# Performance work log

Hardware: AMD Instinct MI355X
Metric: run time of the kernel (lower is better)

## Reference

```python
import jax, jax.numpy as jnp
import numpy as np

WINDOW = 32


def _dilate(mask, iters=5):
    # scipy binary_dilation with default cross structure, `iters` iterations
    m = mask.copy()
    for _ in range(iters):
        d = m.copy()
        d[1:, :] |= m[:-1, :]
        d[:-1, :] |= m[1:, :]
        d[:, 1:] |= m[:, :-1]
        d[:, :-1] |= m[:, 1:]
        m = d
    return m


def _label8(mask):
    # skimage measure.label, default 8-connectivity, via min-label propagation
    h, w = mask.shape
    lab = np.where(mask, np.arange(1, mask.size + 1, dtype=np.int64).reshape(h, w), 0)
    BIG = mask.size + 2
    while True:
        p = np.pad(np.where(mask, lab, BIG), 1, constant_values=BIG)
        m = np.full((h, w), BIG, dtype=np.int64)
        for dy in (-1, 0, 1):
            for dx in (-1, 0, 1):
                m = np.minimum(m, p[1 + dy:1 + dy + h, 1 + dx:1 + dx + w])
        new = np.where(mask, m, 0)
        if np.array_equal(new, lab):
            break
        lab = new
    u = np.unique(lab)
    out = np.searchsorted(u, lab)
    if u[0] != 0:
        out = out + 1
    return out


def _malis(seg_flat, e1, e2, costs, pos):
    # MALIS edge weights: Kruskal on descending affinities with union-find;
    # pos=True counts same-(nonzero)-label pairs merged by each edge,
    # pos=False counts cross-label pairs between labeled nodes.
    n = seg_flat.size
    parent = np.arange(n)
    cnt = [dict() for _ in range(n)]
    for i in range(n):
        s = int(seg_flat[i])
        if s != 0:
            cnt[i][s] = 1
    w = np.zeros(costs.shape[0], np.float32)

    def find(x):
        r = x
        while parent[r] != r:
            r = parent[r]
        while parent[x] != r:
            parent[x], x = r, parent[x]
        return r

    order = np.argsort(-costs, kind='stable')
    for ei in order:
        ra, rb = find(int(e1[ei])), find(int(e2[ei]))
        if ra == rb:
            continue
        ca, cb = cnt[ra], cnt[rb]
        small, large = (ca, cb) if len(ca) <= len(cb) else (cb, ca)
        same = 0
        for kk, v in small.items():
            same += v * large.get(kk, 0)
        if pos:
            w[ei] = same
        else:
            sa = sum(ca.values())
            sb = sum(cb.values())
            w[ei] = sa * sb - same
        parent[rb] = ra
        for kk, v in cb.items():
            ca[kk] = ca.get(kk, 0) + v
        cnt[rb] = None
    return w


def compute_malis_weights(pred_np, target_np):
    B, C, H, W = pred_np.shape
    wn_full = np.zeros(pred_np.shape, np.float32)
    wp_full = np.zeros(pred_np.shape, np.float32)
    win = WINDOW
    idx = np.arange(win * win).reshape(win, win)
    e1 = np.concatenate([idx[:, :-1].ravel(), idx[:-1, :].ravel()])
    e2 = np.concatenate([idx[:, 1:].ravel(), idx[1:, :].ravel()])
    for k in range(H // win):
        for j in range(W // win):
            p = pred_np[:, :, k * win:(k + 1) * win, j * win:(j + 1) * win]
            t = target_np[:, :, k * win:(k + 1) * win, j * win:(j + 1) * win]
            costs = np.concatenate([
                (p[:, :, :, :-1] + p[:, :, :, 1:]).reshape(B, -1),
                (p[:, :, :-1, :] + p[:, :, 1:, :]).reshape(B, -1)], axis=1).astype(np.float32)
            gtc = np.concatenate([
                (t[:, :, :, :-1] + t[:, :, :, 1:]).reshape(B, -1),
                (t[:, :, :-1, :] + t[:, :, 1:, :]).reshape(B, -1)], axis=1).astype(np.float32)
            costs_n = costs.copy()
            costs_p = costs.copy()
            costs_n[gtc > 20] = 20
            costs_p[gtc < 10] = 0
            gtc = np.minimum(gtc, 20)
            for i in range(B):
                sg = _label8(_dilate(t[i, 0] == 0, 5) == 0)
                en = _malis(sg.ravel(), e1, e2, costs_n[i], False)
                ep = _malis(sg.ravel(), e1, e2, costs_p[i], True)
                sn = en.sum()
                if sn > 0:
                    en = en / sn
                sp = ep.sum()
                if sp > 0:
                    ep = ep / sp
                en[gtc[i] >= 10] = 0
                ep[gtc[i] < 20] = 0
                for ew, out in ((en, wn_full), (ep, wp_full)):
                    wh, wv = np.split(ew, 2)
                    wh = wh.reshape(win, win - 1)
                    wv = wv.reshape(win - 1, win)
                    nodes = np.zeros((win, win), np.float32)
                    nodes[:, :-1] += wh
                    nodes[:, 1:] += wh
                    nodes[:-1, :] += wv
                    nodes[1:, :] += wv
                    out[i, 0, k * win:(k + 1) * win, j * win:(j + 1) * win] = nodes
    return wn_full, wp_full


def setup_inputs() -> dict:
    key = jax.random.key(0)
    k1, k2 = jax.random.split(key)
    pred = jax.random.uniform(k1, (2, 1, 256, 256), jnp.float32) * 20.0
    target = jax.random.randint(k2, (2, 1, 256, 256), 0, 26).astype(jnp.float32)
    return {"pred": pred, "target": target, "malis_lr": 1.0, "malis_lr_pos": 1.0}


def reference(pred, target, malis_lr, malis_lr_pos):
    # weights are computed from detached values (CPU graph algorithm), constants wrt autodiff
    wn, wp = compute_malis_weights(np.asarray(pred), np.asarray(target))
    wn = jnp.asarray(wn, jnp.float32)
    wp = jnp.asarray(wp, jnp.float32)
    loss = malis_lr * jnp.square(pred) * wn + malis_lr_pos * jnp.square(20.0 - pred) * wp
    return loss.sum()
```

## Files before the change

### kernel.cpp

```cpp
#include <hip/hip_runtime.h>
#include <cstdint>

#define NPIX  1024
#define NH    992
#define NEDGE 1984
#define NSORT 2048
#define NGRP  31
#define HFS   4300
#define POOLN (NPIX + 2*HFS)

typedef unsigned long long u64;
typedef unsigned int u32;

static __device__ __forceinline__ u64 packRoot(int sL,int off,int len,int cap){
    return (u64)(u32)(sL & 0x7FF) | ((u64)(u32)(off & 0x3FFF) << 11) |
           ((u64)(u32)(len & 0x7FF) << 25) | ((u64)(u32)(cap & 0x7FF) << 36);
}
#define R_SL(R)  ((int)((R) & 0x7FF))
#define R_OFF(R) ((int)(((R)>>11) & 0x3FFF))
#define R_LEN(R) ((int)(((R)>>25) & 0x7FF))
#define R_CAP(R) ((int)(((R)>>36) & 0x7FF))
#define EMASK 0x3FFFFFFu

static __device__ __forceinline__ int rdl(int v, int l){ return __builtin_amdgcn_readlane(v, l); }

static __device__ __forceinline__ u64 sxor64(u64 v, int m){
    u32 lo = (u32)__shfl_xor((int)(v & 0xFFFFFFFFull), m, 64);
    u32 hi = (u32)__shfl_xor((int)(v >> 32), m, 64);
    return ((u64)hi << 32) | lo;
}

static __device__ __forceinline__ void edgeAB(int e, int &a, int &b){
    if (e < NH) { int r = (int)((unsigned)e / 31u); a = e + r; b = a + 1; }
    else        { a = e - NH; b = a + 32; }
}

#define CE(x, y, up) { u64 _a=(x), _b=(y); bool _lt=(_a<_b); \
    u64 _mn=_lt?_a:_b, _mx=_lt?_b:_a; (x)=(up)?_mn:_mx; (y)=(up)?_mx:_mn; }
#define CEX(x, xm, keepmin) { u64 _p=sxor64((x),(xm)); bool _lt=((x)<_p); \
    u64 _mn=_lt?(x):_p, _mx=_lt?_p:(x); (x)=(keepmin)?_mn:_mx; }

static __device__ __forceinline__ int wredi(int v){
    #pragma unroll
    for (int o = 32; o > 0; o >>= 1) v += __shfl_xor(v, o, 64);
    return v;
}
static __device__ __forceinline__ float wredf(float v){
    #pragma unroll
    for (int o = 32; o > 0; o >>= 1) v += __shfl_xor(v, o, 64);
    return v;
}

__global__ __launch_bounds__(128) void malis_kernel(
    const float* __restrict__ pred,
    const float* __restrict__ target,
    const float* __restrict__ lr_p,
    const float* __restrict__ lrp_p,
    float* __restrict__ out)
{
    const int tid  = threadIdx.x;
    const int lane = tid & 63;
    const int wv   = tid >> 6;
    const int bid  = blockIdx.x;
    const int bb   = bid >> 6;
    const int win  = bid & 63;
    const int wy   = win >> 3, wx = win & 7;
    const int base = bb * 65536 + (wy * 32) * 256 + wx * 32;

    __shared__ __align__(16) u32 Ks[2][NSORT];
    __shared__ u64   root[2][NPIX];
    __shared__ float predL[NPIX];
    __shared__ float costs[NEDGE];
    __shared__ u32   poolS[2][POOLN];
    __shared__ unsigned short Q[2][NPIX];
    __shared__ float Qw[2][NPIX];
    __shared__ u32   claimS[2][NPIX];
    __shared__ short seg[NPIX];
    __shared__ short par[2][NPIX];
    __shared__ short H[2][NPIX + 1];
    __shared__ unsigned char tgtL[NPIX];
    __shared__ unsigned char gtcL[NEDGE];
    __shared__ u32   rowmaskL[32];
    __shared__ u32   fgL[32];
    __shared__ unsigned short baseL[33];
    __shared__ int   flags[2];

    u32* runPar = (u32*)poolS;
    unsigned short* labIdRun = (unsigned short*)(runPar + 512);

    for (int j = 0; j < 8; ++j) {
        int i = tid + 128 * j;
        int r = i >> 5, c = i & 31;
        float pv = pred[base + r * 256 + c];
        float tv = target[base + r * 256 + c];
        predL[i] = pv;
        tgtL[i]  = (unsigned char)tv;
        u64 zb = __ballot(tv == 0.0f);
        if (lane == 0) {
            int rr = 4 * j + 2 * wv;
            rowmaskL[rr]     = (u32)zb;
            rowmaskL[rr + 1] = (u32)(zb >> 32);
        }
    }
    if (tid == 0) flags[1] = 0;
    for (int x = tid; x < 512; x += 128) runPar[x] = (u32)x;
    __syncthreads();

    if (tid < 32) {
        u32 m = rowmaskL[tid];
        #pragma unroll
        for (int it = 0; it < 5; ++it) {
            u32 um = __shfl(m, (tid == 0) ? 0 : tid - 1, 64);
            if (tid == 0) um = 0;
            u32 dm = __shfl(m, (tid == 31) ? 31 : tid + 1, 64);
            if (tid == 31) dm = 0;
            m = m | (m << 1) | (m >> 1) | um | dm;
        }
        u32 f = ~m;
        fgL[tid] = f;
        int ns = __popc(f & ~(f << 1));
        int x = ns;
        #pragma unroll
        for (int off = 1; off < 32; off <<= 1) {
            int y = __shfl(x, (tid >= off) ? tid - off : 0, 64);
            if (tid >= off) x += y;
        }
        baseL[tid] = (unsigned short)(x - ns);
        if (tid == 31) baseL[32] = (unsigned short)x;
    }
    __syncthreads();
    const int nRuns = (int)baseL[32];

    for (;;) {
        if (tid == 0) flags[0] = 0;
        __syncthreads();
        bool chg = false;
        for (int j = 0; j < 8; ++j) {
            int i = tid + 128 * j;
            int r = i >> 5, c = i & 31;
            if (r == 0) continue;
            u32 fr = fgL[r];
            if (!((fr >> c) & 1u)) continue;
            u32 fu = fgL[r - 1];
            u32 nb = fu & (u32)((7ull << c) >> 1);
            if (!nb) continue;
            u32 Sr = fr & ~(fr << 1);
            int a = (int)baseL[r] + __popc(Sr & ((2u << c) - 1u)) - 1;
            for (;;) { int p = (int)runPar[a]; if (p == a) break; a = p; }
            u32 Su = fu & ~(fu << 1);
            int bu = (int)baseL[r - 1];
            while (nb) {
                int cc = __ffs((int)nb) - 1; nb &= nb - 1;
                int b = bu + __popc(Su & ((2u << cc) - 1u)) - 1;
                for (;;) { int p = (int)runPar[b]; if (p == b) break; b = p; }
                if (a != b) {
                    int mnr = a < b ? a : b;
                    int mxr = a ^ b ^ mnr;
                    atomicMin(&runPar[mxr], (u32)mnr);
                    chg = true;
                    a = mnr;
                }
            }
        }
        if (chg) flags[0] = 1;
        __syncthreads();
        if (!flags[0]) break;
        for (int x = tid; x < nRuns; x += 128) {
            u32 p = runPar[x];
            runPar[x] = runPar[p];
        }
        __syncthreads();
    }

    for (int x = tid; x < nRuns; x += 128)
        if ((int)runPar[x] == x) labIdRun[x] = (unsigned short)atomicAdd(&flags[1], 1);
    __syncthreads();

    for (int j = 0; j < 8; ++j) {
        int i = tid + 128 * j;
        int r = i >> 5, c = i & 31;
        u32 fr = fgL[r];
        short s = 0;
        if ((fr >> c) & 1u) {
            u32 Sr = fr & ~(fr << 1);
            int x = (int)baseL[r] + __popc(Sr & ((2u << c) - 1u)) - 1;
            for (;;) { int p = (int)runPar[x]; if (p == x) break; x = p; }
            s = (short)((int)labIdRun[x] + 1);
        }
        seg[i] = s;
    }

    for (int e = tid; e < NEDGE; e += 128) {
        int a, b2; edgeAB(e, a, b2);
        costs[e] = predL[a] + predL[b2];
        gtcL[e]  = (unsigned char)(tgtL[a] + tgtL[b2]);
    }
    __syncthreads();

    const int ph = wv;
    u32*   Ks_   = Ks[ph];
    short* par_  = par[ph];
    u64*   root_ = root[ph];
    u32*   pool_ = poolS[ph];
    short* H_    = H[ph];
    unsigned short* Q_ = Q[ph];
    float* Qw_   = Qw[ph];
    u32*   claim_= claimS[ph];

    u64 sk[32];
    #pragma unroll
    for (int r = 0; r < 32; ++r) {
        int e = lane * 32 + r;
        u64 kv = ~0ULL;
        if (e < NEDGE) {
            float cv = costs[e];
            int g = gtcL[e];
            if (ph == 0) { if (g > 20) cv = 20.0f; }
            else         { if (g < 10) cv = 0.0f; }
            kv = (((u64)(~__float_as_uint(cv))) << 32) | (u32)e;
        }
        sk[r] = kv;
    }
    #pragma unroll
    for (int kk2 = 2; kk2 <= 32; kk2 <<= 1) {
        #pragma unroll
        for (int j = kk2 >> 1; j > 0; j >>= 1) {
            #pragma unroll
            for (int r = 0; r < 32; ++r) {
                if ((r & j) == 0) {
                    bool up = (kk2 == 32) ? ((lane & 1) == 0) : ((r & kk2) == 0);
                    CE(sk[r], sk[r | j], up);
                }
            }
        }
    }
    #pragma unroll
    for (int kk2 = 64; kk2 <= 2048; kk2 <<= 1) {
        const bool up = ((lane & (kk2 >> 5)) == 0);
        #pragma unroll
        for (int j = kk2 >> 1; j >= 32; j >>= 1) {
            const int xm = j >> 5;
            const bool keepmin = (((lane & xm) == 0) == up);
            #pragma unroll
            for (int r = 0; r < 32; ++r) { CEX(sk[r], xm, keepmin); }
        }
        #pragma unroll
        for (int j = 16; j > 0; j >>= 1) {
            #pragma unroll
            for (int r = 0; r < 32; ++r) {
                if ((r & j) == 0) { CE(sk[r], sk[r | j], up); }
            }
        }
    }
    #pragma unroll
    for (int r = 0; r < 32; r += 4) {
        uint4 v4;
        v4.x = (u32)sk[r]; v4.y = (u32)sk[r+1]; v4.z = (u32)sk[r+2]; v4.w = (u32)sk[r+3];
        *(uint4*)&Ks_[lane * 32 + r] = v4;
    }

    for (int i = lane; i < NPIX; i += 64) {
        short s2 = seg[i];
        par_[i] = (short)(i | (s2 ? 0x8000 : 0));
        root_[i] = s2 ? ((1ull << 62) | ((u32)(unsigned short)s2 << 16) | 1u) : 0ull;
        H_[i] = 0;
        claim_[i] = ~0u;
    }
    if (lane == 0) H_[NPIX] = 0;
    __builtin_amdgcn_wave_barrier();

    const u64 ltm = (1ull << lane) - 1;
    u32 bump = NPIX;
    u32 halfEnd = NPIX + HFS;
    int curHalf = 0;

    auto do_gc = [&]() {
        u32 tgt = (curHalf == 0) ? (u32)(NPIX + HFS) : (u32)NPIX;
        u32 nb = tgt;
        for (int c = 0; c < 16; ++c) {
            int i0 = c * 64 + lane;
            u64 Ri = root_[i0];
            bool live = (Ri != 0) && ((Ri >> 62) == 0);
            u64 rbm = __ballot(live);
            while (rbm) {
                int j = __ffsll(rbm) - 1; rbm &= rbm - 1;
                int r = c * 64 + j;
                u64 R = root_[r];
                int len = R_LEN(R);
                int off = R_OFF(R);
                for (int t = lane; t < len; t += 64) {
                    u32 v2 = pool_[off + t];
                    pool_[nb + t] = v2;
                }
                __builtin_amdgcn_wave_barrier();
                if (lane == 0) root_[r] = packRoot(R_SL(R), (int)nb, len, len);
                nb += (u32)len;
            }
        }
        bump = nb;
        halfEnd = tgt + HFS;
        curHalf ^= 1;
    };

    int qn = 0;
    u32 rnd = 1;
    int curE = (int)Ks_[lane];
    for (int g2 = 0; g2 < NGRP; ++g2) {
        int nextE = (g2 + 1 < NGRP) ? (int)Ks_[(g2 + 1) * 64 + lane] : 0;
        const int myE = curE;
        int ea, eb2; edgeAB(myE, ea, eb2);
        int ra = ea, rb = eb2;
        int laA, laB;
        for (;;) {
            int va = (int)(unsigned short)par_[ra];
            int vb = (int)(unsigned short)par_[rb];
            int pa = va & 0x3FF, pb = vb & 0x3FF;
            bool fa = (pa != ra), fb = (pb != rb);
            if (!fa && !fb) { laA = va >> 15; laB = vb >> 15; break; }
            int ga = (int)(unsigned short)par_[pa];
            int gb = (int)(unsigned short)par_[pb];
            if (fa) { par_[ra] = (short)ga; ra = ga & 0x3FF; }
            if (fb) { par_[rb] = (short)gb; rb = gb & 0x3FF; }
        }
        bool alive = (ra != rb);

        for (;;) {
            if (!__ballot(alive)) break;
            const bool av = alive;
            const u32 tag = ((0x03FFFFFFu - rnd) << 6) | (u32)lane;
            ++rnd;
            int mn = ra < rb ? ra : rb;
            int mx = ra ^ rb ^ mn;
            int winner = (laA == laB) ? mn : (laA ? ra : rb);
            int loser  = (laA == laB) ? mx : (laA ? rb : ra);
            bool wgt = (laA & laB) != 0;
            if (av)        atomicMin(&claim_[loser],  tag);
            if (av && wgt) atomicMin(&claim_[winner], tag);
            bool sel = false;
            if (av) {
                u32 cl = claim_[loser];
                u32 cw = wgt ? claim_[winner] : tag;
                sel = (cl == tag) && (cw == tag);
            }
            u64 wm = __ballot(sel && wgt);
            int qidx = qn + (int)__popcll(wm & ltm);
            qn += (int)__popcll(wm);
            if (sel) par_[loser] = (short)winner;

            bool needPool = false;
            if (sel && wgt) {
                u64 RW = root_[mn], RL = root_[mx];
                int tW = (int)(RW >> 62), tL2 = (int)(RL >> 62);
                if (tW != 0 && tL2 != 0) {
                    u32 a0 = (u32)RW & EMASK, a1 = (u32)(RW >> 26) & EMASK;
                    u32 b0 = (u32)RL & EMASK, b1 = (u32)(RL >> 26) & EMASK;
                    u32 la0 = a0 >> 16, la1 = a1 >> 16;
                    u32 lb0 = b0 >> 16, lb1 = b1 >> 16;
                    int ca0 = (int)(a0 & 0xFFFF), ca1 = (int)(a1 & 0xFFFF);
                    int cb0 = (int)(b0 & 0xFFFF), cb1 = (int)(b1 & 0xFFFF);
                    int sLa = ca0 + ((tW == 2) ? ca1 : 0);
                    int sLb = cb0 + ((tL2 == 2) ? cb1 : 0);
                    int same = 0;
                    if (lb0 == la0) same += ca0 * cb0;
                    else if (tW == 2 && lb0 == la1) same += ca1 * cb0;
                    if (tL2 == 2) {
                        if (lb1 == la0) same += ca0 * cb1;
                        else if (tW == 2 && lb1 == la1) same += ca1 * cb1;
                    }
                    u32 r0 = a0, r1 = (tW == 2) ? a1 : 0;
                    int n = tW; bool ovf = false;
                    if (lb0 == la0) r0 += (u32)cb0;
                    else if (tW == 2 && lb0 == la1) r1 += (u32)cb0;
                    else { if (n == 1) { r1 = b0; n = 2; } else ovf = true; }
                    if (tL2 == 2) {
                        if (lb1 == la0) r0 += (u32)cb1;
                        else if (tW == 2 && lb1 == la1) r1 += (u32)cb1;
                        else { if (n == 1) { r1 = b1; n = 2; } else ovf = true; }
                    }
                    if (!ovf) {
                        root_[mn] = ((u64)(u32)n << 62) | ((u64)r1 << 26) | r0;
                        root_[mx] = 0;
                        Qw_[qidx] = (float)(ph ? same : (sLa * sLb - same));
                        Q_[qidx]  = (unsigned short)myE;
                    } else needPool = true;
                } else needPool = true;
            }

            u64 pm = __ballot(needPool);
            while (pm) {
                int f = __ffsll(pm) - 1; pm &= pm - 1;
                int A  = rdl(mn, f),  B  = rdl(mx, f);
                int e  = rdl(myE, f), qi = rdl(qidx, f);
                u64 RA = root_[A], RB = root_[B];
                int tA = (int)(RA >> 62), tB = (int)(RB >> 62);
                int lenA = tA ? tA : R_LEN(RA);
                int lenB = tB ? tB : R_LEN(RB);
                if (bump + (u32)(lenA + lenB + 8) > halfEnd) {
                    do_gc();
                    RA = root_[A]; RB = root_[B];
                    tA = (int)(RA >> 62); tB = (int)(RB >> 62);
                    lenA = tA ? tA : R_LEN(RA);
                    lenB = tB ? tB : R_LEN(RB);
                }
                int sLa, sLb;
                int offA = 0, capA = 0, offB = 0, capB = 0;
                if (tA == 0) { sLa = R_SL(RA); offA = R_OFF(RA); capA = R_CAP(RA); }
                else {
                    u32 a0 = (u32)RA & EMASK, a1 = (u32)(RA >> 26) & EMASK;
                    sLa = (int)(a0 & 0xFFFF) + ((tA == 2) ? (int)(a1 & 0xFFFF) : 0);
                }
                if (tB == 0) { sLb = R_SL(RB); offB = R_OFF(RB); capB = R_CAP(RB); }
                else {
                    u32 b0 = (u32)RB & EMASK, b1 = (u32)(RB >> 26) & EMASK;
                    sLb = (int)(b0 & 0xFFFF) + ((tB == 2) ? (int)(b1 & 0xFFFF) : 0);
                }
                u32 eA = 0, eB = 0;
                if (lenA <= 64) {
                    if (tA == 0) { if (lane < lenA) eA = pool_[offA + lane]; }
                    else {
                        u32 a0 = (u32)RA & EMASK, a1 = (u32)(RA >> 26) & EMASK;
                        eA = (lane == 0) ? a0 : ((lane == 1 && tA == 2) ? a1 : 0);
                    }
                }
                if (lenB <= 64) {
                    if (tB == 0) { if (lane < lenB) eB = pool_[offB + lane]; }
                    else {
                        u32 b0 = (u32)RB & EMASK, b1 = (u32)(RB >> 26) & EMASK;
                        eB = (lane == 0) ? b0 : ((lane == 1 && tB == 2) ? b1 : 0);
                    }
                }
                u32 eS, eL; int lenS, lenL, offS, offL, capL, tL;
                if (lenA <= lenB) { eS=eA; lenS=lenA; offS=offA; eL=eB; lenL=lenB; offL=offB; capL=capB; tL=tB; }
                else              { eS=eB; lenS=lenB; offS=offB; eL=eA; lenL=lenA; offL=offA; capL=capA; tL=tA; }
                int dOff, dLen, dCap;
                int same = 0;
                u64 newR;

                if (lenS + lenL <= 64) {
                    dLen = lenL;
                    for (int t = 0; t < lenS; ++t) {
                        u32 xs = (u32)rdl((int)eS, t);
                        bool match = (lane < lenL) && ((eL >> 16) == (xs >> 16));
                        u64 mb = __ballot(match);
                        if (mb) {
                            int ml = __ffsll(mb) - 1;
                            same += (int)(xs & 0xFFFF) * ((int)rdl((int)eL, ml) & 0xFFFF);
                            if (match) eL += (xs & 0xFFFF);
                        } else {
                            if (lane == dLen) eL = xs;
                            dLen++;
                        }
                    }
                    if (dLen <= 2) {
                        u32 m0 = (u32)rdl((int)eL, 0) & EMASK;
                        u32 m1 = (dLen > 1) ? ((u32)rdl((int)eL, 1) & EMASK) : 0u;
                        newR = ((u64)(u32)dLen << 62) | ((u64)m1 << 26) | m0;
                    } else {
                        if (tL == 0 && dLen <= capL) { dOff = offL; dCap = capL; }
                        else { dOff = (int)bump; dCap = (dLen + 3) & ~3; bump += (u32)dCap; }
                        if (lane < dLen) pool_[dOff + lane] = eL;
                        newR = packRoot(sLa + sLb, dOff, dLen, dCap);
                    }
                } else {
                    dOff = (int)bump;
                    dCap = (lenL + lenS + 4) & ~3; bump += (u32)dCap;
                    if (lenS <= 64) {
                        if (lane < lenS) H_[eS >> 16] = (short)(eS & 0xFFFF);
                    } else {
                        for (int j = lane; j < lenS; j += 64) {
                            u32 es = pool_[offS + j];
                            H_[es >> 16] = (short)(es & 0xFFFF);
                        }
                    }
                    __builtin_amdgcn_wave_barrier();
                    int sp = 0;
                    for (int j = lane; j < lenL; j += 64) {
                        u32 el = pool_[offL + j];
                        int h = (int)H_[el >> 16];
                        sp += h * (int)(el & 0xFFFF);
                        pool_[dOff + j] = el + (u32)h;
                        if (h) H_[el >> 16] = 0;
                    }
                    same = wredi(sp);
                    __builtin_amdgcn_wave_barrier();
                    int baseU = 0;
                    if (lenS <= 64) {
                        bool un = (lane < lenS) && (H_[eS >> 16] != 0);
                        u64 ub = __ballot(un);
                        if (un) {
                            int pos = __popcll(ub & ltm);
                            pool_[dOff + lenL + pos] = eS;
                            H_[eS >> 16] = 0;
                        }
                        baseU = (int)__popcll(ub);
                    } else {
                        for (int j0 = 0; j0 < lenS; j0 += 64) {
                            int j = j0 + lane;
                            bool un = false; u32 es = 0;
                            if (j < lenS) { es = pool_[offS + j]; un = (H_[es >> 16] != 0); }
                            u64 ub = __ballot(un);
                            if (un) {
                                int pos = __popcll(ub & ltm);
                                pool_[dOff + lenL + baseU + pos] = es;
                                H_[es >> 16] = 0;
                            }
                            baseU += (int)__popcll(ub);
                        }
                    }
                    dLen = lenL + baseU;
                    newR = packRoot(sLa + sLb, dOff, dLen, dCap);
                }
                if (lane == 0) {
                    Qw_[qi] = (float)(ph ? same : (sLa * sLb - same));
                    Q_[qi]  = (unsigned short)e;
                    root_[A] = newR;
                    root_[B] = 0;
                }
                __builtin_amdgcn_wave_barrier();
            }

            if (av) {
                for (;;) {
                    int va = (int)(unsigned short)par_[ra];
                    int vb = (int)(unsigned short)par_[rb];
                    int pa = va & 0x3FF, pb = vb & 0x3FF;
                    bool fa = (pa != ra), fb = (pb != rb);
                    if (!fa && !fb) { laA = va >> 15; laB = vb >> 15; break; }
                    int ga = (int)(unsigned short)par_[pa];
                    int gb = (int)(unsigned short)par_[pb];
                    if (fa) { par_[ra] = (short)ga; ra = ga & 0x3FF; }
                    if (fb) { par_[rb] = (short)gb; rb = gb & 0x3FF; }
                }
                alive = !sel && (ra != rb);
            }
        }
        curE = nextE;
        __builtin_amdgcn_wave_barrier();
    }

    float s_loc = 0.0f;
    for (int q = lane; q < qn; q += 64) s_loc += Qw_[q];
    const float sn = wredf(s_loc);

    const float scale = ph ? lrp_p[0] : lr_p[0];
    float acc = 0.0f;
    for (int q = lane; q < qn; q += 64) {
        float wv2 = Qw_[q];
        if (wv2 == 0.0f) continue;
        if (sn > 0.0f) wv2 /= sn;
        int me = (int)Q_[q];
        int g = gtcL[me];
        bool zero = ph ? (g < 20) : (g >= 10);
        if (zero) continue;
        int a2, b2; edgeAB(me, a2, b2);
        float pa = predL[a2], pb = predL[b2];
        float fa2, fb2;
        if (ph == 0) { fa2 = pa * pa; fb2 = pb * pb; }
        else { float qa = 20.0f - pa, qb = 20.0f - pb; fa2 = qa * qa; fb2 = qb * qb; }
        acc += scale * wv2 * (fa2 + fb2);
    }
    acc = wredf(acc);
    if (lane == 0) atomicAdd(out, acc);
}

__global__ void zero_out_kernel(float* o)
{
    if (threadIdx.x == 0 && blockIdx.x == 0) o[0] = 0.0f;
}

extern "C" void kernel_launch(void* const* d_in, const int* in_sizes, int n_in,
                              void* d_out, int out_size, void* d_ws, size_t ws_size,
                              hipStream_t stream)
{
    const float* pred   = (const float*)d_in[0];
    const float* target = (const float*)d_in[1];
    const float* lr     = (const float*)d_in[2];
    const float* lrp    = (const float*)d_in[3];
    float* out = (float*)d_out;

    zero_out_kernel<<<1, 64, 0, stream>>>(out);
    malis_kernel<<<128, 128, 0, stream>>>(pred, target, lr, lrp, out);
}
```

Measured before the change: 322.4 us.

## Split MALIS kernel into preprocessing and per-phase drain kernels

Splits the monolithic kernel into a pre_kernel that labels segments and sorts edges per window, writing them to workspace, and a drain_kernel that runs each Kruskal phase (pos/neg) in its own 64-thread block. This doubles the number of blocks (256 instead of 128) so the serial union-find phases spread over more CUs, and reduces per-block LDS. In exchange it adds a kernel launch and a global-memory round trip for labels and sorted keys. The drain reads sorted keys from global rather than LDS.

```diff
diff --git a/kernel.cpp b/kernel.cpp
--- a/kernel.cpp
+++ b/kernel.cpp
@@ -12,6 +12,9 @@
 typedef unsigned long long u64;
 typedef unsigned int u32;
 
+#define WS_SEG   0
+#define WS_KS    262144
+
 static __device__ __forceinline__ u64 packRoot(int sL,int off,int len,int cap){
     return (u64)(u32)(sL & 0x7FF) | ((u64)(u32)(off & 0x3FFF) << 11) |
            ((u64)(u32)(len & 0x7FF) << 25) | ((u64)(u32)(cap & 0x7FF) << 36);
@@ -35,6 +38,13 @@
     else        { a = e - NH; b = a + 32; }
 }
 
+static __device__ __forceinline__ int winBase(int wslot){
+    int bb = wslot >> 6;
+    int win = wslot & 63;
+    int wy = win >> 3, wx = win & 7;
+    return bb * 65536 + (wy * 32) * 256 + wx * 32;
+}
+
 #define CE(x, y, up) { u64 _a=(x), _b=(y); bool _lt=(_a<_b); \
     u64 _mn=_lt?_a:_b, _mx=_lt?_b:_a; (x)=(up)?_mn:_mx; (y)=(up)?_mx:_mn; }
 #define CEX(x, xm, keepmin) { u64 _p=sxor64((x),(xm)); bool _lt=((x)<_p); \
@@ -51,42 +61,28 @@
     return v;
 }
 
-__global__ __launch_bounds__(128) void malis_kernel(
+__global__ __launch_bounds__(128) void pre_kernel(
     const float* __restrict__ pred,
     const float* __restrict__ target,
-    const float* __restrict__ lr_p,
-    const float* __restrict__ lrp_p,
-    float* __restrict__ out)
+    unsigned short* __restrict__ segW,
+    u32* __restrict__ KsW)
 {
     const int tid  = threadIdx.x;
     const int lane = tid & 63;
     const int wv   = tid >> 6;
     const int bid  = blockIdx.x;
-    const int bb   = bid >> 6;
-    const int win  = bid & 63;
-    const int wy   = win >> 3, wx = win & 7;
-    const int base = bb * 65536 + (wy * 32) * 256 + wx * 32;
-
-    __shared__ __align__(16) u32 Ks[2][NSORT];
-    __shared__ u64   root[2][NPIX];
+    const int base = winBase(bid);
+
     __shared__ float predL[NPIX];
     __shared__ float costs[NEDGE];
-    __shared__ u32   poolS[2][POOLN];
-    __shared__ unsigned short Q[2][NPIX];
-    __shared__ float Qw[2][NPIX];
-    __shared__ u32   claimS[2][NPIX];
-    __shared__ short seg[NPIX];
-    __shared__ short par[2][NPIX];
-    __shared__ short H[2][NPIX + 1];
     __shared__ unsigned char tgtL[NPIX];
     __shared__ unsigned char gtcL[NEDGE];
     __shared__ u32   rowmaskL[32];
     __shared__ u32   fgL[32];
     __shared__ unsigned short baseL[33];
+    __shared__ u32   runPar[512];
+    __shared__ unsigned short labIdRun[512];
     __shared__ int   flags[2];
-
-    u32* runPar = (u32*)poolS;
-    unsigned short* labIdRun = (unsigned short*)(runPar + 512);
 
     for (int j = 0; j < 8; ++j) {
         int i = tid + 128 * j;
@@ -176,18 +172,19 @@
         if ((int)runPar[x] == x) labIdRun[x] = (unsigned short)atomicAdd(&flags[1], 1);
     __syncthreads();
 
+    unsigned short* segG = segW + bid * NPIX;
     for (int j = 0; j < 8; ++j) {
         int i = tid + 128 * j;
         int r = i >> 5, c = i & 31;
         u32 fr = fgL[r];
-        short s = 0;
+        unsigned short s = 0;
         if ((fr >> c) & 1u) {
             u32 Sr = fr & ~(fr << 1);
             int x = (int)baseL[r] + __popc(Sr & ((2u << c) - 1u)) - 1;
             for (;;) { int p = (int)runPar[x]; if (p == x) break; x = p; }
-            s = (short)((int)labIdRun[x] + 1);
-        }
-        seg[i] = s;
+            s = (unsigned short)((int)labIdRun[x] + 1);
+        }
+        segG[i] = s;
     }
 
     for (int e = tid; e < NEDGE; e += 128) {
@@ -198,15 +195,6 @@
     __syncthreads();
 
     const int ph = wv;
-    u32*   Ks_   = Ks[ph];
-    short* par_  = par[ph];
-    u64*   root_ = root[ph];
-    u32*   pool_ = poolS[ph];
-    short* H_    = H[ph];
-    unsigned short* Q_ = Q[ph];
-    float* Qw_   = Qw[ph];
-    u32*   claim_= claimS[ph];
-
     u64 sk[32];
     #pragma unroll
     for (int r = 0; r < 32; ++r) {
@@ -252,21 +240,59 @@
             }
         }
     }
+    u32* KsG = KsW + (size_t)(bid * 2 + ph) * NSORT;
     #pragma unroll
     for (int r = 0; r < 32; r += 4) {
         uint4 v4;
         v4.x = (u32)sk[r]; v4.y = (u32)sk[r+1]; v4.z = (u32)sk[r+2]; v4.w = (u32)sk[r+3];
-        *(uint4*)&Ks_[lane * 32 + r] = v4;
-    }
+        *(uint4*)&KsG[lane * 32 + r] = v4;
+    }
+}
+
+__global__ __launch_bounds__(64) void drain_kernel(
+    const float* __restrict__ pred,
+    const float* __restrict__ target,
+    const unsigned short* __restrict__ segW,
+    const u32* __restrict__ KsW,
+    const float* __restrict__ lr_p,
+    const float* __restrict__ lrp_p,
+    float* __restrict__ out)
+{
+    const int lane = threadIdx.x;
+    const int bid  = blockIdx.x;
+    const int ph   = bid & 1;
+    const int wslot= bid >> 1;
+    const int base = winBase(wslot);
+    const unsigned short* segG = segW + wslot * NPIX;
+    const u32* KsG = KsW + (size_t)bid * NSORT;
+
+    __shared__ u64   root_[NPIX];
+    __shared__ u32   pool_[POOLN];
+    __shared__ unsigned short Q_[NPIX];
+    __shared__ float Qw_[NPIX];
+    __shared__ u32   claim_[NPIX];
+    __shared__ short par_[NPIX];
+    __shared__ short H_[NPIX + 1];
+    __shared__ float predL[NPIX];
+    __shared__ unsigned char tgtL[NPIX];
+    __shared__ unsigned char gtcL[NEDGE];
 
     for (int i = lane; i < NPIX; i += 64) {
-        short s2 = seg[i];
+        int r = i >> 5, c = i & 31;
+        predL[i] = pred[base + r * 256 + c];
+        tgtL[i]  = (unsigned char)target[base + r * 256 + c];
+        unsigned short s2 = segG[i];
         par_[i] = (short)(i | (s2 ? 0x8000 : 0));
-        root_[i] = s2 ? ((1ull << 62) | ((u32)(unsigned short)s2 << 16) | 1u) : 0ull;
+        root_[i] = s2 ? ((1ull << 62) | ((u32)s2 << 16) | 1u) : 0ull;
         H_[i] = 0;
         claim_[i] = ~0u;
     }
     if (lane == 0) H_[NPIX] = 0;
+    __builtin_amdgcn_wave_barrier();
+    for (int e = lane; e < NEDGE; e += 64) {
+        int a, b2; edgeAB(e, a, b2);
+        gtcL[e] = (unsigned char)(tgtL[a] + tgtL[b2]);
+    }
     __builtin_amdgcn_wave_barrier();
 
     const u64 ltm = (1ull << lane) - 1;
@@ -304,9 +330,9 @@
 
     int qn = 0;
     u32 rnd = 1;
-    int curE = (int)Ks_[lane];
+    int curE = (int)KsG[lane];
     for (int g2 = 0; g2 < NGRP; ++g2) {
-        int nextE = (g2 + 1 < NGRP) ? (int)Ks_[(g2 + 1) * 64 + lane] : 0;
+        int nextE = (g2 + 1 < NGRP) ? (int)KsG[(g2 + 1) * 64 + lane] : 0;
         const int myE = curE;
         int ea, eb2; edgeAB(myE, ea, eb2);
         int ra = ea, rb = eb2;
@@ -578,6 +604,11 @@
     const float* lrp    = (const float*)d_in[3];
     float* out = (float*)d_out;
 
+    char* ws = (char*)d_ws;
+    unsigned short* segW = (unsigned short*)(ws + WS_SEG);
+    u32* KsW = (u32*)(ws + WS_KS);
+
     zero_out_kernel<<<1, 64, 0, stream>>>(out);
-    malis_kernel<<<128, 128, 0, stream>>>(pred, target, lr, lrp, out);
-}
+    pre_kernel<<<128, 128, 0, stream>>>(pred, target, segW, KsW);
+    drain_kernel<<<256, 64, 0, stream>>>(pred, target, segW, KsW, lr, lrp, out);
+}
```

Result: slower. 331.6 us (+2.9%).

## Split pos/neg MALIS phases into separate single-wave blocks

Applied to the files above, without the earlier changes.

Each 128-thread block previously ran both phases (one per wave) after a shared labeling preamble; now each phase runs in its own 64-thread block, giving 256 blocks. The labeling preamble uses wave barriers and ballots instead of __syncthreads and shared flags, with label ids assigned by ballot prefix counts. This spreads work across more CUs and removes block-level syncs, but the labeling and edge-cost preamble is now computed twice per window by a single wave.

```diff
diff --git a/kernel.cpp b/kernel.cpp
--- a/kernel.cpp
+++ b/kernel.cpp
@@ -35,6 +35,13 @@
     else        { a = e - NH; b = a + 32; }
 }
 
+static __device__ __forceinline__ int winBase(int wslot){
+    int bb = wslot >> 6;
+    int win = wslot & 63;
+    int wy = win >> 3, wx = win & 7;
+    return bb * 65536 + (wy * 32) * 256 + wx * 32;
+}
+
 #define CE(x, y, up) { u64 _a=(x), _b=(y); bool _lt=(_a<_b); \
     u64 _mn=_lt?_a:_b, _mx=_lt?_b:_a; (x)=(up)?_mn:_mx; (y)=(up)?_mx:_mn; }
 #define CEX(x, xm, keepmin) { u64 _p=sxor64((x),(xm)); bool _lt=((x)<_p); \
@@ -51,92 +58,85 @@
     return v;
 }
 
-__global__ __launch_bounds__(128) void malis_kernel(
+__global__ __launch_bounds__(64) void malis_kernel(
     const float* __restrict__ pred,
     const float* __restrict__ target,
     const float* __restrict__ lr_p,
     const float* __restrict__ lrp_p,
     float* __restrict__ out)
 {
-    const int tid  = threadIdx.x;
-    const int lane = tid & 63;
-    const int wv   = tid >> 6;
+    const int lane = threadIdx.x;
     const int bid  = blockIdx.x;
-    const int bb   = bid >> 6;
-    const int win  = bid & 63;
-    const int wy   = win >> 3, wx = win & 7;
-    const int base = bb * 65536 + (wy * 32) * 256 + wx * 32;
-
-    __shared__ __align__(16) u32 Ks[2][NSORT];
-    __shared__ u64   root[2][NPIX];
+    const int ph   = bid & 1;
+    const int wslot= bid >> 1;
+    const int base = winBase(wslot);
+    const u64 ltm = (1ull << lane) - 1;
+
+    __shared__ __align__(16) u32 Ks_[NSORT];
+    __shared__ u64   root_[NPIX];
+    __shared__ u32   pool_[POOLN];
+    __shared__ unsigned short Q_[NPIX];
+    __shared__ float Qw_[NPIX];
+    __shared__ u32   claim_[NPIX];
+    __shared__ short par_[NPIX];
+    __shared__ short H_[NPIX + 1];
     __shared__ float predL[NPIX];
     __shared__ float costs[NEDGE];
-    __shared__ u32   poolS[2][POOLN];
-    __shared__ unsigned short Q[2][NPIX];
-    __shared__ float Qw[2][NPIX];
-    __shared__ u32   claimS[2][NPIX];
     __shared__ short seg[NPIX];
-    __shared__ short par[2][NPIX];
-    __shared__ short H[2][NPIX + 1];
     __shared__ unsigned char tgtL[NPIX];
     __shared__ unsigned char gtcL[NEDGE];
     __shared__ u32   rowmaskL[32];
     __shared__ u32   fgL[32];
     __shared__ unsigned short baseL[33];
-    __shared__ int   flags[2];
-
-    u32* runPar = (u32*)poolS;
+
+    u32* runPar = (u32*)pool_;
     unsigned short* labIdRun = (unsigned short*)(runPar + 512);
 
-    for (int j = 0; j < 8; ++j) {
-        int i = tid + 128 * j;
-        int r = i >> 5, c = i & 31;
+    for (int j = 0; j < 16; ++j) {
+        int i = lane + 64 * j;
+        int r = (j << 1) + (lane >> 5), c = lane & 31;
         float pv = pred[base + r * 256 + c];
         float tv = target[base + r * 256 + c];
         predL[i] = pv;
         tgtL[i]  = (unsigned char)tv;
         u64 zb = __ballot(tv == 0.0f);
         if (lane == 0) {
-            int rr = 4 * j + 2 * wv;
-            rowmaskL[rr]     = (u32)zb;
-            rowmaskL[rr + 1] = (u32)(zb >> 32);
-        }
-    }
-    if (tid == 0) flags[1] = 0;
-    for (int x = tid; x < 512; x += 128) runPar[x] = (u32)x;
-    __syncthreads();
-
-    if (tid < 32) {
-        u32 m = rowmaskL[tid];
+            rowmaskL[2*j]     = (u32)zb;
+            rowmaskL[2*j + 1] = (u32)(zb >> 32);
+        }
+    }
+    for (int x = lane; x < 512; x += 64) runPar[x] = (u32)x;
+    __builtin_amdgcn_wave_barrier();
+
+    if (lane < 32) {
+        u32 m = rowmaskL[lane];
         #pragma unroll
         for (int it = 0; it < 5; ++it) {
-            u32 um = __shfl(m, (tid == 0) ? 0 : tid - 1, 64);
-            if (tid == 0) um = 0;
-            u32 dm = __shfl(m, (tid == 31) ? 31 : tid + 1, 64);
-            if (tid == 31) dm = 0;
+            u32 um = __shfl(m, (lane == 0) ? 0 : lane - 1, 64);
+            if (lane == 0) um = 0;
+            u32 dm = __shfl(m, (lane == 31) ? 31 : lane + 1, 64);
+            if (lane == 31) dm = 0;
             m = m | (m << 1) | (m >> 1) | um | dm;
         }
         u32 f = ~m;
-        fgL[tid] = f;
+        fgL[lane] = f;
         int ns = __popc(f & ~(f << 1));
         int x = ns;
         #pragma unroll
         for (int off = 1; off < 32; off <<= 1) {
-            int y = __shfl(x, (tid >= off) ? tid - off : 0, 64);
-            if (tid >= off) x += y;
-        }
-        baseL[tid] = (unsigned short)(x - ns);
-        if (tid == 31) baseL[32] = (unsigned short)x;
-    }
-    __syncthreads();
+            int y = __shfl(x, (lane >= off) ? lane - off : 0, 64);
+            if (lane >= off) x += y;
+        }
+        baseL[lane] = (unsigned short)(x - ns);
+        if (lane == 31) baseL[32] = (unsigned short)x;
+    }
+    __builtin_amdgcn_wave_barrier();
     const int nRuns = (int)baseL[32];
 
     for (;;) {
-        if (tid == 0) flags[0] = 0;
-        __syncthreads();
         bool chg = false;
-        for (int j = 0; j < 8; ++j) {
-            int i = tid + 128 * j;
+        for (int j = 0; j < 16; ++j) {
+            int i = lane + 64 * j;
             int r = i >> 5, c = i & 31;
             if (r == 0) continue;
             u32 fr = fgL[r];
@@ -162,22 +162,28 @@
                 }
             }
         }
-        if (chg) flags[0] = 1;
-        __syncthreads();
-        if (!flags[0]) break;
-        for (int x = tid; x < nRuns; x += 128) {
+        if (!__ballot(chg)) break;
+        for (int x = lane; x < nRuns; x += 64) {
             u32 p = runPar[x];
             runPar[x] = runPar[p];
         }
-        __syncthreads();
-    }
-
-    for (int x = tid; x < nRuns; x += 128)
-        if ((int)runPar[x] == x) labIdRun[x] = (unsigned short)atomicAdd(&flags[1], 1);
-    __syncthreads();
-
-    for (int j = 0; j < 8; ++j) {
-        int i = tid + 128 * j;
+        __builtin_amdgcn_wave_barrier();
+    }
+
+    {
+        int kacc = 0;
+        for (int x0 = 0; x0 < nRuns; x0 += 64) {
+            int x = x0 + lane;
+            bool isr = (x < nRuns) && ((int)runPar[x] == x);
+            u64 bm = __ballot(isr);
+            if (isr) labIdRun[x] = (unsigned short)(kacc + (int)__popcll(bm & ltm));
+            kacc += (int)__popcll(bm);
+        }
+    }
+    __builtin_amdgcn_wave_barrier();
+
+    for (int j = 0; j < 16; ++j) {
+        int i = lane + 64 * j;
         int r = i >> 5, c = i & 31;
         u32 fr = fgL[r];
         short s = 0;
@@ -190,22 +196,12 @@
         seg[i] = s;
     }
 
-    for (int e = tid; e < NEDGE; e += 128) {
+    for (int e = lane; e < NEDGE; e += 64) {
         int a, b2; edgeAB(e, a, b2);
         costs[e] = predL[a] + predL[b2];
         gtcL[e]  = (unsigned char)(tgtL[a] + tgtL[b2]);
     }
-    __syncthreads();
-
-    const int ph = wv;
-    u32*   Ks_   = Ks[ph];
-    short* par_  = par[ph];
-    u64*   root_ = root[ph];
-    u32*   pool_ = poolS[ph];
-    short* H_    = H[ph];
-    unsigned short* Q_ = Q[ph];
-    float* Qw_   = Qw[ph];
-    u32*   claim_= claimS[ph];
+    __builtin_amdgcn_wave_barrier();
 
     u64 sk[32];
     #pragma unroll
@@ -269,7 +265,6 @@
     if (lane == 0) H_[NPIX] = 0;
     __builtin_amdgcn_wave_barrier();
 
-    const u64 ltm = (1ull << lane) - 1;
     u32 bump = NPIX;
     u32 halfEnd = NPIX + HFS;
     int curHalf = 0;
@@ -579,5 +574,5 @@
     float* out = (float*)d_out;
 
     zero_out_kernel<<<1, 64, 0, stream>>>(out);
-    malis_kernel<<<128, 128, 0, stream>>>(pred, target, lr, lrp, out);
-}
+    malis_kernel<<<256, 64, 0, stream>>>(pred, target, lr, lrp, out);
+}
```

New measurement: 323.9 us. No clear change (+0.5%).
